# Optimization experiments

Measured on AMD Instinct MI355X. Metric: run time of the kernel, lower is better.

Reference implementation:

```python
import jax, jax.numpy as jnp
import numpy as np

N = 100000
E = 1600000
IN_FEATS = 256
OUT_FEATS = 256
EPS_WSUM = 1e-8   # clamp for weight sum
EPS_NORM = 1e-12  # F.normalize eps


def setup_inputs() -> dict:
    key = jax.random.key(0)
    k1, k2, k3, k4, k5 = jax.random.split(key, 5)
    x = jax.random.normal(k1, (N, IN_FEATS), dtype=jnp.float32)
    edge_index = jax.random.randint(k2, (2, E), 0, N, dtype=jnp.int64)
    edge_weight = jax.random.uniform(k3, (E,), dtype=jnp.float32)
    # Xavier-uniform-like init scale for [out, in] weights
    lim = float(np.sqrt(6.0 / (IN_FEATS + OUT_FEATS)) * np.sqrt(2.0))
    W_self = jax.random.uniform(k4, (OUT_FEATS, IN_FEATS), dtype=jnp.float32, minval=-lim, maxval=lim)
    W_neigh = jax.random.uniform(k5, (OUT_FEATS, IN_FEATS), dtype=jnp.float32, minval=-lim, maxval=lim)
    bias = jnp.zeros((OUT_FEATS,), dtype=jnp.float32)
    return {"x": x, "edge_index": edge_index, "edge_weight": edge_weight,
            "W_self": W_self, "W_neigh": W_neigh, "bias": bias}


def reference(x, edge_index, edge_weight, W_self, W_neigh, bias):
    row, col = edge_index[0], edge_index[1]
    # weighted mean aggregation: gather -> scale -> scatter-add -> normalize by weight sum
    weighted = x[row] * edge_weight[:, None]                       # [E, in]
    num = jax.ops.segment_sum(weighted, col, num_segments=N)       # [N, in]
    wsum = jax.ops.segment_sum(edge_weight, col, num_segments=N)   # [N]
    wsum = jnp.maximum(wsum, EPS_WSUM)
    neigh = num / wsum[:, None]                                    # [N, in]
    out = x @ W_self.T + neigh @ W_neigh.T + bias                  # [N, out]
    # L2 normalize (torch F.normalize semantics)
    nrm = jnp.maximum(jnp.linalg.norm(out, axis=-1, keepdims=True), EPS_NORM)
    return out / nrm
```

## Files before the change

### kernel.cpp

```cpp
#include <hip/hip_runtime.h>
#include <hip/hip_bf16.h>
#include <stdint.h>

#define IN_F 256
#define K_TOT 512
#define GR 64

typedef __attribute__((ext_vector_type(8))) _Float16 f16x8;
typedef __attribute__((ext_vector_type(4))) _Float16 f16x4;
typedef __attribute__((ext_vector_type(4))) float f32x4;
typedef __attribute__((ext_vector_type(2))) float f32x2;

#if __has_builtin(__builtin_amdgcn_cvt_pk_f32_fp8) && __has_builtin(__builtin_amdgcn_cvt_pk_fp8_f32)
#define HW_FP8 1
#endif

__device__ __forceinline__ float fp8_dec1(uint32_t b) {
  union { uint16_t u; _Float16 h; } cv;
  cv.u = (uint16_t)((b & 0x7F) << 7);
  float v = (float)cv.h * 256.0f;
  return (b & 0x80) ? -v : v;
}
__device__ __forceinline__ uint32_t fp8_enc1(float f) {
  union { _Float16 h; uint16_t u; } cv;
  cv.h = (_Float16)(f * (1.0f / 256.0f));
  uint32_t s = (cv.u >> 8) & 0x80;
  uint32_t t = cv.u & 0x7FFF;
  uint32_t r = (t + 0x3F + ((t >> 7) & 1)) >> 7;
  if (r > 0x7E) r = 0x7E;
  return s | r;
}
__device__ __forceinline__ void fp8x4_dec(uint32_t w, float4& o) {
#ifdef HW_FP8
  f32x2 lo = __builtin_amdgcn_cvt_pk_f32_fp8((int)w, false);
  f32x2 hi = __builtin_amdgcn_cvt_pk_f32_fp8((int)w, true);
  o.x = lo[0]; o.y = lo[1]; o.z = hi[0]; o.w = hi[1];
#else
  o.x = fp8_dec1(w & 0xFF); o.y = fp8_dec1((w >> 8) & 0xFF);
  o.z = fp8_dec1((w >> 16) & 0xFF); o.w = fp8_dec1(w >> 24);
#endif
}
__device__ __forceinline__ uint32_t fp8x4_enc(float a, float b, float c, float d) {
#ifdef HW_FP8
  int r = __builtin_amdgcn_cvt_pk_fp8_f32(a, b, 0, false);
  r = __builtin_amdgcn_cvt_pk_fp8_f32(c, d, r, true);
  return (uint32_t)r;
#else
  return fp8_enc1(a) | (fp8_enc1(b) << 8) | (fp8_enc1(c) << 16) | (fp8_enc1(d) << 24);
#endif
}

__global__ void init_kernel(const float* __restrict__ x,
                            const float* __restrict__ Ws,
                            const float* __restrict__ Wn,
                            const int* __restrict__ ei,
                            _Float16* __restrict__ Bhi,
                            uint32_t* __restrict__ xq, _Float16* __restrict__ Af16,
                            int* __restrict__ counts,
                            int* __restrict__ flag, int N, int E,
                            int nconv, int nhist) {
  __shared__ int bad_s[256];
  const int b = blockIdx.x;
  const int t = threadIdx.x;
  if (b < 512) {
    int idx = b * 256 + t;
    int j = idx >> 9;
    int k = idx & 511;
    float v = (k < IN_F) ? Ws[j * IN_F + k] : Wn[j * IN_F + (k - IN_F)];
    size_t addr = ((size_t)(k >> 5) * 256 + j) * 32 + (k & 31);
    Bhi[addr] = (_Float16)v;
  } else if (b < 512 + nconv + nhist) {
    int m = b - 512;
    int npair = 2 * (nconv < nhist ? nconv : nhist);
    int role, ci;
    if (m < npair) { role = m & 1; ci = m >> 1; }
    else if (nconv > nhist) { role = 0; ci = nhist + (m - npair); }
    else { role = 1; ci = nconv + (m - npair); }
    if (role == 0) {
      size_t base = (size_t)ci * 4096 + (size_t)t * 16;
      size_t tot = (size_t)N * IN_F;
      if (base + 16 <= tot) {
        const float4* x4 = reinterpret_cast<const float4*>(x + base);
        float4 v0 = x4[0], v1 = x4[1], v2 = x4[2], v3 = x4[3];
        uint4 o;
        o.x = fp8x4_enc(v0.x, v0.y, v0.z, v0.w);
        o.y = fp8x4_enc(v1.x, v1.y, v1.z, v1.w);
        o.z = fp8x4_enc(v2.x, v2.y, v2.z, v2.w);
        o.w = fp8x4_enc(v3.x, v3.y, v3.z, v3.w);
        *reinterpret_cast<uint4*>(xq + base / 4) = o;
        size_t row = base >> 8;
        int col = (int)(base & 255);
        f16x8 h0 = {(_Float16)v0.x, (_Float16)v0.y, (_Float16)v0.z, (_Float16)v0.w,
                    (_Float16)v1.x, (_Float16)v1.y, (_Float16)v1.z, (_Float16)v1.w};
        f16x8 h1 = {(_Float16)v2.x, (_Float16)v2.y, (_Float16)v2.z, (_Float16)v2.w,
                    (_Float16)v3.x, (_Float16)v3.y, (_Float16)v3.z, (_Float16)v3.w};
        _Float16* dst = Af16 + row * K_TOT + col;
        *reinterpret_cast<f16x8*>(dst) = h0;
        *reinterpret_cast<f16x8*>(dst + 8) = h1;
      }
    } else {
      int bad = 0;
#pragma unroll
      for (int p = 0; p < 8; ++p)
        if (ei[2 * (t + p * 256) + 1] != 0) bad = 1;
      bad_s[t] = bad;
      __syncthreads();
      for (int s = 128; s > 0; s >>= 1) {
        if (t < s) bad_s[t] |= bad_s[t + s];
        __syncthreads();
      }
      int is64 = (bad_s[0] == 0);
      int e = ci * 256 + t;
      if (e < E) {
        int dst = is64 ? ei[2 * (E + e)] : ei[E + e];
        atomicAdd(counts + dst, 1);
      }
    }
  } else {
    int bad = 0;
#pragma unroll
    for (int p = 0; p < 8; ++p) {
      int i = t + p * 256;
      if (ei[2 * i + 1] != 0) bad = 1;
    }
    bad_s[t] = bad;
    __syncthreads();
    for (int s = 128; s > 0; s >>= 1) {
      if (t < s) bad_s[t] |= bad_s[t + s];
      __syncthreads();
    }
    if (t == 0) *flag = (bad_s[0] == 0) ? 1 : 0;
  }
}

__global__ void scan1_kernel(const int* __restrict__ counts, int* __restrict__ offsets,
                             int* __restrict__ bsums, int N) {
  __shared__ int buf[1024];
  int t = threadIdx.x;
  int i = blockIdx.x * 1024 + t;
  int v = (i < N) ? counts[i] : 0;
  buf[t] = v;
  __syncthreads();
  for (int s = 1; s < 1024; s <<= 1) {
    int add = (t >= s) ? buf[t - s] : 0;
    __syncthreads();
    buf[t] += add;
    __syncthreads();
  }
  if (i < N) offsets[i] = buf[t] - v;
  if (t == 1023) bsums[blockIdx.x] = buf[1023];
}

__global__ void scan23_kernel(int* __restrict__ offsets, const int* __restrict__ bsums,
                              int* __restrict__ cursor, int N, int E, int nb) {
  __shared__ int sb[128];
  int t = threadIdx.x;
  int v = 0;
  if (t < 128) {
    v = (t < nb) ? bsums[t] : 0;
    sb[t] = v;
  }
  __syncthreads();
  for (int s = 1; s < 128; s <<= 1) {
    int add = 0;
    if (t < 128 && t >= s) add = sb[t - s];
    __syncthreads();
    if (t < 128) sb[t] += add;
    __syncthreads();
  }
  if (t < 128) sb[t] -= v;
  __syncthreads();
  int i = blockIdx.x * 256 + t;
  if (i < N) {
    int o = offsets[i] + sb[i >> 10];
    offsets[i] = o;
    cursor[i] = o;
  }
  if (i == 0) offsets[N] = E;
}

__global__ void fill_kernel(const int* __restrict__ ei, const float* __restrict__ ew,
                            const int* __restrict__ flag, int* __restrict__ cursor,
                            uint32_t* __restrict__ edges, int E, int nper) {
  int q = blockIdx.x & 7;
  int e = (blockIdx.x >> 3) * 256 + threadIdx.x;
  if (e >= E) return;
  int is64 = *flag;
  int dst = is64 ? ei[2 * (E + e)] : ei[E + e];
  if ((unsigned)(dst - q * nper) >= (unsigned)nper) return;
  int src = is64 ? ei[2 * e] : ei[e];
  uint32_t w15 = (uint32_t)__float2int_rn(ew[e] * 32767.0f);
  int pos = atomicAdd(cursor + dst, 1);
  edges[pos] = ((uint32_t)src << 15) | w15;
}

__launch_bounds__(256)
__global__ void aggregate_fp8_kernel(const uint32_t* __restrict__ xq,
                                     const int* __restrict__ offsets,
                                     const uint32_t* __restrict__ edges,
                                     _Float16* __restrict__ Af16, int N) {
  int wid = blockIdx.x * 4 + (threadIdx.x >> 6);
  if (wid >= N) return;
  uint32_t lane = threadIdx.x & 63;
  int beg = offsets[wid];
  int end = offsets[wid + 1];
  float4 acc = {0.f, 0.f, 0.f, 0.f};
  float ws = 0.f;
  const float wscale = 1.0f / 32767.0f;
  int e = beg;
  for (; e + 7 < end; e += 8) {
    uint32_t n[8];
#pragma unroll
    for (int j = 0; j < 8; ++j) n[j] = edges[e + j];
    uint32_t q[8];
#pragma unroll
    for (int j = 0; j < 8; ++j) q[j] = xq[(n[j] >> 15) * 64u + lane];
#pragma unroll
    for (int j = 0; j < 8; ++j) {
      float wj = (float)(n[j] & 0x7FFF) * wscale;
      float4 fj;
      fp8x4_dec(q[j], fj);
      acc.x += fj.x * wj; acc.y += fj.y * wj;
      acc.z += fj.z * wj; acc.w += fj.w * wj;
      ws += wj;
    }
  }
  for (; e < end; ++e) {
    uint32_t n0 = edges[e];
    float w0 = (float)(n0 & 0x7FFF) * wscale;
    uint32_t q0 = xq[(n0 >> 15) * 64u + lane];
    float4 f0;
    fp8x4_dec(q0, f0);
    acc.x += f0.x * w0; acc.y += f0.y * w0; acc.z += f0.z * w0; acc.w += f0.w * w0;
    ws += w0;
  }
  float inv = 1.f / fmaxf(ws, 1e-8f);
  f16x4 o = {(_Float16)(acc.x * inv), (_Float16)(acc.y * inv),
             (_Float16)(acc.z * inv), (_Float16)(acc.w * inv)};
  *reinterpret_cast<f16x4*>(Af16 + (size_t)wid * K_TOT + IN_F + lane * 4) = o;
}

__launch_bounds__(256)
__global__ void gemm_norm_kernel(const _Float16* __restrict__ Af16,
                                 const _Float16* __restrict__ Bhi,
                                 const float* __restrict__ bias,
                                 float* __restrict__ out, int N) {
  const int t = threadIdx.x;
  const int lane = t & 63;
  const int w = t >> 6;
  const int row0 = blockIdx.x * GR;

  __shared__ _Float16 Ah[2][256 * 8];
  __shared__ float ssb[GR][4];

  f32x4 acc[4][4];
#pragma unroll
  for (int rt = 0; rt < 4; ++rt)
#pragma unroll
    for (int ct = 0; ct < 4; ++ct) acc[rt][ct] = (f32x4){0.f, 0.f, 0.f, 0.f};

  int st_row = row0 + (t >> 6) * 16 + (t & 15);
  if (st_row >= N) st_row = N - 1;
  const _Float16* Abase = Af16 + (size_t)st_row * K_TOT + ((t >> 4) & 3) * 8;

  const size_t bfrag = (size_t)(w * 64 + (lane & 15)) * 32 + (lane >> 4) * 8;
  const _Float16* BhiP = Bhi + bfrag;

  *reinterpret_cast<f16x8*>(&Ah[0][t * 8]) = *reinterpret_cast<const f16x8*>(Abase);
  f16x8 a_next = *reinterpret_cast<const f16x8*>(Abase + 32);
  f16x8 bH[2][4];
#pragma unroll
  for (int ct = 0; ct < 4; ++ct) {
    bH[0][ct] = *reinterpret_cast<const f16x8*>(BhiP + ct * 512);
    bH[1][ct] = *reinterpret_cast<const f16x8*>(BhiP + 8192 + ct * 512);
  }
  __syncthreads();

#pragma unroll
  for (int ks = 0; ks < 16; ++ks) {
    f16x8 aH[4];
#pragma unroll
    for (int rt = 0; rt < 4; ++rt)
      aH[rt] = *reinterpret_cast<const f16x8*>(&Ah[ks & 1][(rt * 64 + lane) * 8]);
    f16x8 bNext[4];
    if (ks < 14) {
#pragma unroll
      for (int ct = 0; ct < 4; ++ct)
        bNext[ct] = *reinterpret_cast<const f16x8*>(BhiP + (size_t)(ks + 2) * 8192 + ct * 512);
    }
    if (ks < 15)
      *reinterpret_cast<f16x8*>(&Ah[(ks + 1) & 1][t * 8]) = a_next;
    if (ks < 14)
      a_next = *reinterpret_cast<const f16x8*>(Abase + (size_t)(ks + 2) * 32);
#pragma unroll
    for (int ct = 0; ct < 4; ++ct)
#pragma unroll
      for (int rt = 0; rt < 4; ++rt)
        acc[rt][ct] = __builtin_amdgcn_mfma_f32_16x16x32_f16(aH[rt], bH[ks & 1][ct], acc[rt][ct], 0, 0, 0);
    if (ks < 14) {
#pragma unroll
      for (int ct = 0; ct < 4; ++ct) bH[ks & 1][ct] = bNext[ct];
    }
    __syncthreads();
  }

  float bv[4];
#pragma unroll
  for (int ct = 0; ct < 4; ++ct) bv[ct] = bias[w * 64 + ct * 16 + (lane & 15)];

#pragma unroll
  for (int rt = 0; rt < 4; ++rt)
#pragma unroll
    for (int i = 0; i < 4; ++i) {
      float ssv = 0.f;
#pragma unroll
      for (int ct = 0; ct < 4; ++ct) {
        float val = acc[rt][ct][i] + bv[ct];
        acc[rt][ct][i] = val;
        ssv += val * val;
      }
#pragma unroll
      for (int s = 1; s < 16; s <<= 1) ssv += __shfl_xor(ssv, s, 64);
      if ((lane & 15) == 0) ssb[rt * 16 + (lane >> 4) * 4 + i][w] = ssv;
    }
  __syncthreads();

#pragma unroll
  for (int rt = 0; rt < 4; ++rt)
#pragma unroll
    for (int i = 0; i < 4; ++i) {
      int rl = rt * 16 + (lane >> 4) * 4 + i;
      f32x4 s4 = *reinterpret_cast<const f32x4*>(&ssb[rl][0]);
      float ss = s4[0] + s4[1] + s4[2] + s4[3];
      int gr = row0 + rl;
      if (gr < N) {
        float scale = 1.0f / fmaxf(sqrtf(ss), 1e-12f);
#pragma unroll
        for (int ct = 0; ct < 4; ++ct)
          out[(size_t)gr * IN_F + w * 64 + ct * 16 + (lane & 15)] = acc[rt][ct][i] * scale;
      }
    }
}

extern "C" void kernel_launch(void* const* d_in, const int* in_sizes, int n_in,
                              void* d_out, int out_size, void* d_ws, size_t ws_size,
                              hipStream_t stream) {
  const float* x = (const float*)d_in[0];
  const int* ei = (const int*)d_in[1];
  const float* ew = (const float*)d_in[2];
  const float* Wself = (const float*)d_in[3];
  const float* Wneigh = (const float*)d_in[4];
  const float* bias = (const float*)d_in[5];
  float* out = (float*)d_out;

  const int N = in_sizes[0] / IN_F;
  const int E = in_sizes[2];

  char* p = (char*)d_ws;
  _Float16* Af16 = (_Float16*)p;     p += (size_t)N * K_TOT * 2;
  _Float16* Bhi = (_Float16*)p;      p += (size_t)K_TOT * IN_F * 2;
  uint32_t* xq = (uint32_t*)p;       p += (size_t)N * IN_F;
  uint32_t* edges = (uint32_t*)p;    p += (size_t)E * 4;
  int* counts = (int*)p;             p += (size_t)N * 4;
  int* offsets = (int*)p;            p += (size_t)(N + 1) * 4;
  int* cursor = (int*)p;             p += (size_t)N * 4;
  int* bsums = (int*)p;              p += 128 * 4;
  int* flag = (int*)p;

  const int nconv = (int)(((size_t)N * IN_F + 4095) / 4096);
  const int nhist = (E + 255) / 256;
  const int nb = (N + 1023) / 1024;
  const int nper = (N + 7) / 8;

  hipMemsetAsync(counts, 0, (size_t)N * sizeof(int), stream);

  init_kernel<<<512 + nconv + nhist + 1, 256, 0, stream>>>(
      x, Wself, Wneigh, ei, Bhi, xq, Af16, counts, flag, N, E, nconv, nhist);
  scan1_kernel<<<nb, 1024, 0, stream>>>(counts, offsets, bsums, N);
  scan23_kernel<<<(N + 255) / 256, 256, 0, stream>>>(offsets, bsums, cursor, N, E, nb);
  fill_kernel<<<((E + 255) / 256) * 8, 256, 0, stream>>>(ei, ew, flag, cursor, edges,
                                                         E, nper);
  aggregate_fp8_kernel<<<(N + 3) / 4, 256, 0, stream>>>(xq, offsets, edges, Af16, N);
  gemm_norm_kernel<<<(N + GR - 1) / GR, 256, 0, stream>>>(Af16, Bhi, bias, out, N);
}
```

Baseline: 281.5 us.

## Move x fp8/fp16 conversion from init kernel into fill kernel, interleaved

The conversion of x to fp8 and fp16 no longer runs in the init kernel, which is now weight repacking plus edge-degree histogram only. It moves into a combined fill_conv kernel, where every ninth block does conversion and the other eight do CSR edge fill. The aim is to overlap the bandwidth-bound conversion with the latency-bound, atomic-heavy fill scatter, and to shorten the init stage ahead of the scan. The cost is the extra index arithmetic per block and some sharing of cache and bandwidth between the two workloads.

New measurement: 300.0 us. 1.07x slower.

```diff
diff --git a/kernel.cpp b/kernel.cpp
--- a/kernel.cpp
+++ b/kernel.cpp
@@ -50,15 +50,12 @@
 #endif
 }
 
-__global__ void init_kernel(const float* __restrict__ x,
-                            const float* __restrict__ Ws,
+__global__ void init_kernel(const float* __restrict__ Ws,
                             const float* __restrict__ Wn,
                             const int* __restrict__ ei,
                             _Float16* __restrict__ Bhi,
-                            uint32_t* __restrict__ xq, _Float16* __restrict__ Af16,
                             int* __restrict__ counts,
-                            int* __restrict__ flag, int N, int E,
-                            int nconv, int nhist) {
+                            int* __restrict__ flag, int E, int nhist) {
   __shared__ int bad_s[256];
   const int b = blockIdx.x;
   const int t = threadIdx.x;
@@ -69,52 +66,22 @@
     float v = (k < IN_F) ? Ws[j * IN_F + k] : Wn[j * IN_F + (k - IN_F)];
     size_t addr = ((size_t)(k >> 5) * 256 + j) * 32 + (k & 31);
     Bhi[addr] = (_Float16)v;
-  } else if (b < 512 + nconv + nhist) {
-    int m = b - 512;
-    int npair = 2 * (nconv < nhist ? nconv : nhist);
-    int role, ci;
-    if (m < npair) { role = m & 1; ci = m >> 1; }
-    else if (nconv > nhist) { role = 0; ci = nhist + (m - npair); }
-    else { role = 1; ci = nconv + (m - npair); }
-    if (role == 0) {
-      size_t base = (size_t)ci * 4096 + (size_t)t * 16;
-      size_t tot = (size_t)N * IN_F;
-      if (base + 16 <= tot) {
-        const float4* x4 = reinterpret_cast<const float4*>(x + base);
-        float4 v0 = x4[0], v1 = x4[1], v2 = x4[2], v3 = x4[3];
-        uint4 o;
-        o.x = fp8x4_enc(v0.x, v0.y, v0.z, v0.w);
-        o.y = fp8x4_enc(v1.x, v1.y, v1.z, v1.w);
-        o.z = fp8x4_enc(v2.x, v2.y, v2.z, v2.w);
-        o.w = fp8x4_enc(v3.x, v3.y, v3.z, v3.w);
-        *reinterpret_cast<uint4*>(xq + base / 4) = o;
-        size_t row = base >> 8;
-        int col = (int)(base & 255);
-        f16x8 h0 = {(_Float16)v0.x, (_Float16)v0.y, (_Float16)v0.z, (_Float16)v0.w,
-                    (_Float16)v1.x, (_Float16)v1.y, (_Float16)v1.z, (_Float16)v1.w};
-        f16x8 h1 = {(_Float16)v2.x, (_Float16)v2.y, (_Float16)v2.z, (_Float16)v2.w,
-                    (_Float16)v3.x, (_Float16)v3.y, (_Float16)v3.z, (_Float16)v3.w};
-        _Float16* dst = Af16 + row * K_TOT + col;
-        *reinterpret_cast<f16x8*>(dst) = h0;
-        *reinterpret_cast<f16x8*>(dst + 8) = h1;
-      }
-    } else {
-      int bad = 0;
-#pragma unroll
-      for (int p = 0; p < 8; ++p)
-        if (ei[2 * (t + p * 256) + 1] != 0) bad = 1;
-      bad_s[t] = bad;
+  } else if (b < 512 + nhist) {
+    int bad = 0;
+#pragma unroll
+    for (int p = 0; p < 8; ++p)
+      if (ei[2 * (t + p * 256) + 1] != 0) bad = 1;
+    bad_s[t] = bad;
+    __syncthreads();
+    for (int s = 128; s > 0; s >>= 1) {
+      if (t < s) bad_s[t] |= bad_s[t + s];
       __syncthreads();
-      for (int s = 128; s > 0; s >>= 1) {
-        if (t < s) bad_s[t] |= bad_s[t + s];
-        __syncthreads();
-      }
-      int is64 = (bad_s[0] == 0);
-      int e = ci * 256 + t;
-      if (e < E) {
-        int dst = is64 ? ei[2 * (E + e)] : ei[E + e];
-        atomicAdd(counts + dst, 1);
-      }
+    }
+    int is64 = (bad_s[0] == 0);
+    int e = (b - 512) * 256 + t;
+    if (e < E) {
+      int dst = is64 ? ei[2 * (E + e)] : ei[E + e];
+      atomicAdd(counts + dst, 1);
     }
   } else {
     int bad = 0;
@@ -179,19 +146,53 @@
   if (i == 0) offsets[N] = E;
 }
 
-__global__ void fill_kernel(const int* __restrict__ ei, const float* __restrict__ ew,
-                            const int* __restrict__ flag, int* __restrict__ cursor,
-                            uint32_t* __restrict__ edges, int E, int nper) {
-  int q = blockIdx.x & 7;
-  int e = (blockIdx.x >> 3) * 256 + threadIdx.x;
-  if (e >= E) return;
-  int is64 = *flag;
-  int dst = is64 ? ei[2 * (E + e)] : ei[E + e];
-  if ((unsigned)(dst - q * nper) >= (unsigned)nper) return;
-  int src = is64 ? ei[2 * e] : ei[e];
-  uint32_t w15 = (uint32_t)__float2int_rn(ew[e] * 32767.0f);
-  int pos = atomicAdd(cursor + dst, 1);
-  edges[pos] = ((uint32_t)src << 15) | w15;
+__global__ void fill_conv_kernel(const float* __restrict__ x,
+                                 const int* __restrict__ ei,
+                                 const float* __restrict__ ew,
+                                 const int* __restrict__ flag,
+                                 int* __restrict__ cursor,
+                                 uint32_t* __restrict__ edges,
+                                 uint32_t* __restrict__ xq,
+                                 _Float16* __restrict__ Af16,
+                                 int N, int E, int nper, int nconv) {
+  const int m = blockIdx.x;
+  const int t = threadIdx.x;
+  const int ci = m / 9;
+  if ((m % 9) == 0 && ci < nconv) {
+    size_t base = (size_t)ci * 4096 + (size_t)t * 16;
+    size_t tot = (size_t)N * IN_F;
+    if (base + 16 <= tot) {
+      const float4* x4 = reinterpret_cast<const float4*>(x + base);
+      float4 v0 = x4[0], v1 = x4[1], v2 = x4[2], v3 = x4[3];
+      uint4 o;
+      o.x = fp8x4_enc(v0.x, v0.y, v0.z, v0.w);
+      o.y = fp8x4_enc(v1.x, v1.y, v1.z, v1.w);
+      o.z = fp8x4_enc(v2.x, v2.y, v2.z, v2.w);
+      o.w = fp8x4_enc(v3.x, v3.y, v3.z, v3.w);
+      *reinterpret_cast<uint4*>(xq + base / 4) = o;
+      size_t row = base >> 8;
+      int col = (int)(base & 255);
+      f16x8 h0 = {(_Float16)v0.x, (_Float16)v0.y, (_Float16)v0.z, (_Float16)v0.w,
+                  (_Float16)v1.x, (_Float16)v1.y, (_Float16)v1.z, (_Float16)v1.w};
+      f16x8 h1 = {(_Float16)v2.x, (_Float16)v2.y, (_Float16)v2.z, (_Float16)v2.w,
+                  (_Float16)v3.x, (_Float16)v3.y, (_Float16)v3.z, (_Float16)v3.w};
+      _Float16* dst = Af16 + row * K_TOT + col;
+      *reinterpret_cast<f16x8*>(dst) = h0;
+      *reinterpret_cast<f16x8*>(dst + 8) = h1;
+    }
+  } else if ((m % 9) != 0) {
+    int fi = m - ci - 1;
+    int q = fi & 7;
+    int e = (fi >> 3) * 256 + t;
+    if (e >= E) return;
+    int is64 = *flag;
+    int dst = is64 ? ei[2 * (E + e)] : ei[E + e];
+    if ((unsigned)(dst - q * nper) >= (unsigned)nper) return;
+    int src = is64 ? ei[2 * e] : ei[e];
+    uint32_t w15 = (uint32_t)__float2int_rn(ew[e] * 32767.0f);
+    int pos = atomicAdd(cursor + dst, 1);
+    edges[pos] = ((uint32_t)src << 15) | w15;
+  }
 }
 
 __launch_bounds__(256)
@@ -369,17 +370,18 @@
 
   const int nconv = (int)(((size_t)N * IN_F + 4095) / 4096);
   const int nhist = (E + 255) / 256;
+  const int nfill = nhist * 8;
   const int nb = (N + 1023) / 1024;
   const int nper = (N + 7) / 8;
 
   hipMemsetAsync(counts, 0, (size_t)N * sizeof(int), stream);
 
-  init_kernel<<<512 + nconv + nhist + 1, 256, 0, stream>>>(
-      x, Wself, Wneigh, ei, Bhi, xq, Af16, counts, flag, N, E, nconv, nhist);
+  init_kernel<<<512 + nhist + 1, 256, 0, stream>>>(Wself, Wneigh, ei, Bhi, counts,
+                                                   flag, E, nhist);
   scan1_kernel<<<nb, 1024, 0, stream>>>(counts, offsets, bsums, N);
   scan23_kernel<<<(N + 255) / 256, 256, 0, stream>>>(offsets, bsums, cursor, N, E, nb);
-  fill_kernel<<<((E + 255) / 256) * 8, 256, 0, stream>>>(ei, ew, flag, cursor, edges,
-                                                         E, nper);
+  fill_conv_kernel<<<nfill + nconv, 256, 0, stream>>>(x, ei, ew, flag, cursor, edges,
+                                                      xq, Af16, N, E, nper, nconv);
   aggregate_fp8_kernel<<<(N + 3) / 4, 256, 0, stream>>>(xq, offsets, edges, Af16, N);
   gemm_norm_kernel<<<(N + GR - 1) / GR, 256, 0, stream>>>(Af16, Bhi, bias, out, N);
 }
```
